# Kernel tuning notes

Hardware: AMD Instinct MI355X
Metric: run time of the kernel (lower is better)

## Reference

```python
import jax, jax.numpy as jnp
import numpy as np

D_MODEL = 1024
NUM_HEADS = 16
WINDOW = 128
DEPTH = D_MODEL // NUM_HEADS


def setup_inputs() -> dict:
    key = jax.random.key(0)
    ks = jax.random.split(key, 9)
    B, S = 2, 2048
    scale = 1.0 / np.sqrt(D_MODEL)
    x = jax.random.normal(ks[0], (B, S, D_MODEL), dtype=jnp.float32)
    Wq = jax.random.normal(ks[1], (D_MODEL, D_MODEL), dtype=jnp.float32) * scale
    Wk = jax.random.normal(ks[2], (D_MODEL, D_MODEL), dtype=jnp.float32) * scale
    Wv = jax.random.normal(ks[3], (D_MODEL, D_MODEL), dtype=jnp.float32) * scale
    Wo = jax.random.normal(ks[4], (D_MODEL, D_MODEL), dtype=jnp.float32) * scale
    bq = jnp.zeros((D_MODEL,), jnp.float32)
    bk = jnp.zeros((D_MODEL,), jnp.float32)
    bv = jnp.zeros((D_MODEL,), jnp.float32)
    bo = jnp.zeros((D_MODEL,), jnp.float32)
    return {"x": x, "Wq": Wq, "bq": bq, "Wk": Wk, "bk": bk,
            "Wv": Wv, "bv": bv, "Wo": Wo, "bo": bo}


def _split_heads(t, B, S):
    # [B,S,D] -> [B,H,S,depth]
    return t.reshape(B, S, NUM_HEADS, DEPTH).transpose(0, 2, 1, 3)


def reference(x, Wq, bq, Wk, bk, Wv, bv, Wo, bo):
    B, S, _ = x.shape
    q = _split_heads(x @ Wq + bq, B, S)
    k = _split_heads(x @ Wk + bk, B, S)
    v = _split_heads(x @ Wv + bv, B, S)
    scores = jnp.einsum('bhqd,bhkd->bhqk', q, k) / jnp.sqrt(jnp.float32(DEPTH))
    idx = jnp.arange(S)
    # mask[i_row=j, i_col=i] per original: |i - j| <= window (symmetric)
    local = jnp.abs(idx[None, :] - idx[:, None]) <= WINDOW  # [S,S]
    scores = jnp.where(local[None, None], scores, jnp.float32(-1e9))
    attn = jax.nn.softmax(scores, axis=-1)
    out = jnp.einsum('bhqk,bhkd->bhqd', attn, v)
    concat = out.transpose(0, 2, 1, 3).reshape(B, S, D_MODEL)
    return concat @ Wo + bo
```

## Files before the change

kernel.cpp:

```cpp
#include <hip/hip_runtime.h>
#include <cstdint>
#include <cstddef>

typedef __attribute__((ext_vector_type(8))) short short8;
typedef __attribute__((ext_vector_type(4))) short short4v;
typedef __attribute__((ext_vector_type(4))) float f32x4;
typedef short8 bf16x8;

typedef __attribute__((address_space(1))) const unsigned GU;
typedef __attribute__((address_space(3))) unsigned LU;

__device__ __forceinline__ short f2bf(float f) {
  unsigned u = __builtin_bit_cast(unsigned, f);
  u += 0x7fffu + ((u >> 16) & 1u);
  return (short)(u >> 16);
}

__global__ __launch_bounds__(256) void k_cast_x(const float* __restrict__ x, short* __restrict__ xb) {
  size_t i = ((size_t)blockIdx.x * 256 + threadIdx.x) * 8;
  f32x4 a = *(const f32x4*)(x + i);
  f32x4 b = *(const f32x4*)(x + i + 4);
  short8 o;
#pragma unroll
  for (int j = 0; j < 4; ++j) { o[j] = f2bf(a[j]); o[4 + j] = f2bf(b[j]); }
  *(short8*)(xb + i) = o;
}

__global__ __launch_bounds__(256) void k_tw(const float* __restrict__ W0, const float* __restrict__ W1,
                                            const float* __restrict__ W2, const float* __restrict__ W3,
                                            short* __restrict__ WT) {
  __shared__ short T[64 * 72];
  int bid = blockIdx.x;
  int widx = bid >> 8;
  int t = bid & 255;
  int kr = (t >> 4) * 64, nc = (t & 15) * 64;
  const float* W = widx == 0 ? W0 : widx == 1 ? W1 : widx == 2 ? W2 : W3;
  short* out = WT + (size_t)widx * 1048576;
  int tid = threadIdx.x;
#pragma unroll
  for (int i = 0; i < 4; ++i) {
    int idx = tid + i * 256;
    int k = idx >> 4, n4 = (idx & 15) << 2;
    f32x4 v = *(const f32x4*)(W + (size_t)(kr + k) * 1024 + nc + n4);
#pragma unroll
    for (int j = 0; j < 4; ++j) T[(n4 + j) * 72 + k] = f2bf(v[j]);
  }
  __syncthreads();
#pragma unroll
  for (int i = 0; i < 2; ++i) {
    int idx = tid + i * 256;
    int n = idx >> 3, k8 = (idx & 7) << 3;
    *(short8*)(out + (size_t)(nc + n) * 1024 + kr + k8) = *(const short8*)&T[n * 72 + k8];
  }
}

__global__ __launch_bounds__(256) void k_tv(const short* __restrict__ v, short* __restrict__ vT) {
  __shared__ short T[64 * 72];
  int bid = blockIdx.x;
  int stile = bid & 31, h = (bid >> 5) & 15, b = bid >> 9;
  int s0 = stile * 64;
  int tid = threadIdx.x;
#pragma unroll
  for (int i = 0; i < 2; ++i) {
    int idx = tid + i * 256;
    int s = idx >> 3, d0 = (idx & 7) << 3;
    short8 vec = *(const short8*)(v + ((size_t)b * 2048 + s0 + s) * 1024 + h * 64 + d0);
#pragma unroll
    for (int j = 0; j < 8; ++j) T[(d0 + j) * 72 + s] = vec[j];
  }
  __syncthreads();
#pragma unroll
  for (int i = 0; i < 2; ++i) {
    int idx = tid + i * 256;
    int d = idx >> 3, s8 = (idx & 7) << 3;
    *(short8*)(vT + (((size_t)b * 16 + h) * 64 + d) * 2048 + s0 + s8) = *(const short8*)&T[d * 72 + s8];
  }
}

__global__ __launch_bounds__(512, 2) void k_gemm256(
    const short* __restrict__ A, const short* __restrict__ BT,
    const float* __restrict__ bias0, const float* __restrict__ bias1, const float* __restrict__ bias2,
    short* __restrict__ outb) {
  __shared__ short S[65536];
  const int tid = threadIdx.x;
  const int lane = tid & 63, w = tid >> 6;
  const int g = lane >> 4, qi = lane & 15;
  const int wm = w >> 2, wn = w & 3;
  int bid = blockIdx.x;
  int swz = (bid & 7) * 24 + (bid >> 3);
  const int tm = swz / 12, tn = swz % 12;
  const int m0 = tm * 256, n0 = tn * 256;
  const size_t K = 1024;
  const short* Ab = A + (size_t)m0 * K;
  const short* Bb = BT + (size_t)n0 * K;

  auto stage = [&](int roff, const short* gbase, int kt) {
#pragma unroll
    for (int i = 0; i < 2; ++i) {
      int cc = tid + i * 512;
      int r = cc >> 3;
      int js = ((cc & 7) ^ (r & 7)) << 3;
      __builtin_amdgcn_global_load_lds((GU*)(gbase + (size_t)r * K + kt * 64 + js),
                                       (LU*)(&S[roff + cc * 8]), 16, 0, 0);
    }
  };
  auto lda = [&](int roff, int row, int kk) -> bf16x8 {
    return *(const bf16x8*)&S[roff + row * 64 + (((kk * 4 + g) ^ (row & 7)) << 3)];
  };

  f32x4 acc[8][4];
#pragma unroll
  for (int i = 0; i < 8; ++i)
#pragma unroll
    for (int j = 0; j < 4; ++j) acc[i][j] = (f32x4)(0.0f);

#define MFA(mi, ni, av, bv) \
  acc[mi][ni] = __builtin_amdgcn_mfma_f32_16x16x32_bf16(av, bv, acc[mi][ni], 0, 0, 0)
#define MF16(Aa, Bb_, o) \
  MFA((o)+0,0,(Aa)[(o)+0],(Bb_)[0]); MFA((o)+0,1,(Aa)[(o)+0],(Bb_)[1]); \
  MFA((o)+0,2,(Aa)[(o)+0],(Bb_)[2]); MFA((o)+0,3,(Aa)[(o)+0],(Bb_)[3]); \
  MFA((o)+1,0,(Aa)[(o)+1],(Bb_)[0]); MFA((o)+1,1,(Aa)[(o)+1],(Bb_)[1]); \
  MFA((o)+1,2,(Aa)[(o)+1],(Bb_)[2]); MFA((o)+1,3,(Aa)[(o)+1],(Bb_)[3]); \
  MFA((o)+2,0,(Aa)[(o)+2],(Bb_)[0]); MFA((o)+2,1,(Aa)[(o)+2],(Bb_)[1]); \
  MFA((o)+2,2,(Aa)[(o)+2],(Bb_)[2]); MFA((o)+2,3,(Aa)[(o)+2],(Bb_)[3]); \
  MFA((o)+3,0,(Aa)[(o)+3],(Bb_)[0]); MFA((o)+3,1,(Aa)[(o)+3],(Bb_)[1]); \
  MFA((o)+3,2,(Aa)[(o)+3],(Bb_)[2]); MFA((o)+3,3,(Aa)[(o)+3],(Bb_)[3])
#define SB __builtin_amdgcn_sched_barrier(0)
#define PHASE_TAIL(MFMAS) do { \
    SB; \
    __builtin_amdgcn_s_barrier(); \
    asm volatile("s_waitcnt lgkmcnt(0)" ::: "memory"); \
    SB; \
    __builtin_amdgcn_s_setprio(1); \
    MFMAS; \
    __builtin_amdgcn_s_setprio(0); \
    SB; \
    __builtin_amdgcn_s_barrier(); \
  } while (0)

  stage(0,     Ab,          0);
  stage(8192,  Ab + 131072, 0);
  stage(16384, Bb,          0);
  stage(24576, Bb + 131072, 0);
  stage(49152, Bb,          1);
  stage(57344, Bb + 131072, 1);
  asm volatile("s_waitcnt vmcnt(4)" ::: "memory");
  __builtin_amdgcn_s_barrier();

  for (int t = 0; t < 16; ++t) {
    const int b = t & 1, nb = b ^ 1;
    const int rA = b * 32768 + wm * 8192;
    const int rB = b * 32768 + 16384 + (wn >> 1) * 8192;
    const int brow = (wn & 1) * 64;
    const int t1 = t + 1 < 15 ? t + 1 : 15;
    const int t2 = t + 2 < 15 ? t + 2 : 15;
    bf16x8 aA[8], aB[4], cA[8], cB[4];

#pragma unroll
    for (int mf = 0; mf < 4; ++mf) aA[mf] = lda(rA, mf * 16 + qi, 0);
#pragma unroll
    for (int nf = 0; nf < 4; ++nf) aB[nf] = lda(rB, brow + nf * 16 + qi, 0);
    stage(nb * 32768, Ab, t1);
    PHASE_TAIL(MF16(aA, aB, 0));
#pragma unroll
    for (int mf = 4; mf < 8; ++mf) aA[mf] = lda(rA, mf * 16 + qi, 0);
#pragma unroll
    for (int nf = 0; nf < 4; ++nf) cB[nf] = lda(rB, brow + nf * 16 + qi, 1);
    stage(nb * 32768 + 8192, Ab + 131072, t1);
    PHASE_TAIL(MF16(aA, aB, 4));
#pragma unroll
    for (int mf = 0; mf < 4; ++mf) cA[mf] = lda(rA, mf * 16 + qi, 1);
    stage(b * 32768 + 16384, Bb, t2);
    PHASE_TAIL(MF16(cA, cB, 0));
#pragma unroll
    for (int mf = 4; mf < 8; ++mf) cA[mf] = lda(rA, mf * 16 + qi, 1);
    stage(b * 32768 + 24576, Bb + 131072, t2);
    asm volatile("s_waitcnt vmcnt(4)" ::: "memory");
    PHASE_TAIL(MF16(cA, cB, 4));
  }
#undef PHASE_TAIL
#undef MF16
#undef MFA
#undef SB

  asm volatile("s_waitcnt vmcnt(0)" ::: "memory");
  __syncthreads();
  int sel = n0 >> 10;
  const float* bias = sel == 0 ? bias0 : (sel == 1 ? bias1 : bias2);
  size_t outoff = (size_t)sel * 4194304;
  int ncol0 = n0 & 1023;
  float bv[4];
#pragma unroll
  for (int nf = 0; nf < 4; ++nf) bv[nf] = bias[ncol0 + wn * 64 + nf * 16 + qi];
  short* Ep = S;
#pragma unroll
  for (int p = 0; p < 2; ++p) {
    __syncthreads();
    if (wm == p) {
#pragma unroll
      for (int mf = 0; mf < 8; ++mf)
#pragma unroll
        for (int nf = 0; nf < 4; ++nf)
#pragma unroll
          for (int j = 0; j < 4; ++j)
            Ep[(mf * 16 + g * 4 + j) * 264 + wn * 64 + nf * 16 + qi] =
                f2bf(acc[mf][nf][j] + bv[nf]);
    }
    __syncthreads();
#pragma unroll
    for (int i = 0; i < 8; ++i) {
      int idx = tid + i * 512;
      int r = idx >> 5, c8 = (idx & 31) << 3;
      int grow = m0 + p * 128 + r;
      *(short8*)&outb[outoff + (size_t)grow * 1024 + ncol0 + c8] = *(const short8*)&Ep[r * 264 + c8];
    }
  }
}

__global__ __launch_bounds__(256, 2) void k_gemmO(
    const short* __restrict__ A, const short* __restrict__ BT,
    const float* __restrict__ bias0, float* __restrict__ outf) {
  __shared__ short Smem[16384];
  const int tid = threadIdx.x;
  const int lane = tid & 63, w = tid >> 6;
  const int g = lane >> 4, qi = lane & 15;
  const int wr = (w >> 1) * 64, wc = (w & 1) * 64;
  const int m0 = blockIdx.y * 128, n0 = blockIdx.x * 128;
  const size_t K = 1024;
  const short* Ab = A + (size_t)m0 * K;
  const short* Bb = BT + (size_t)n0 * K;

  auto stage = [&](int buf, int k0) {
    short* Asb = Smem + buf * 4096;
    short* Bsb = Smem + 8192 + buf * 4096;
#pragma unroll
    for (int i = 0; i < 2; ++i) {
      int cidx = tid + i * 256;
      int r = cidx >> 2;
      int csw = ((cidx & 3) ^ ((r >> 1) & 3)) << 3;
      __builtin_amdgcn_global_load_lds((GU*)(Ab + (size_t)r * K + k0 + csw),
                                       (LU*)(&Asb[cidx * 8]), 16, 0, 0);
      __builtin_amdgcn_global_load_lds((GU*)(Bb + (size_t)r * K + k0 + csw),
                                       (LU*)(&Bsb[cidx * 8]), 16, 0, 0);
    }
  };

  f32x4 acc[4][4];
#pragma unroll
  for (int i = 0; i < 4; ++i)
#pragma unroll
    for (int j = 0; j < 4; ++j) acc[i][j] = (f32x4)(0.0f);

  stage(0, 0);
  __syncthreads();
  for (int kt = 0; kt < 32; ++kt) {
    int cur = kt & 1;
    if (kt < 31) stage(cur ^ 1, (kt + 1) * 32);
    const short* Asb = Smem + cur * 4096;
    const short* Bsb = Smem + 8192 + cur * 4096;
    bf16x8 a[4], b[4];
#pragma unroll
    for (int mf = 0; mf < 4; ++mf) {
      int R = wr + mf * 16 + qi;
      a[mf] = *(const bf16x8*)&Asb[R * 32 + ((g ^ ((R >> 1) & 3)) << 3)];
    }
#pragma unroll
    for (int nf = 0; nf < 4; ++nf) {
      int R = wc + nf * 16 + qi;
      b[nf] = *(const bf16x8*)&Bsb[R * 32 + ((g ^ ((R >> 1) & 3)) << 3)];
    }
#pragma unroll
    for (int mf = 0; mf < 4; ++mf)
#pragma unroll
      for (int nf = 0; nf < 4; ++nf)
        acc[mf][nf] = __builtin_amdgcn_mfma_f32_16x16x32_bf16(a[mf], b[nf], acc[mf][nf], 0, 0, 0);
    __syncthreads();
  }

  float* Ft = (float*)Smem;
  float bv[4];
#pragma unroll
  for (int nf = 0; nf < 4; ++nf) bv[nf] = bias0[n0 + wc + nf * 16 + qi];
#pragma unroll
  for (int mf = 0; mf < 4; ++mf) {
    __syncthreads();
#pragma unroll
    for (int nf = 0; nf < 4; ++nf)
#pragma unroll
      for (int j = 0; j < 4; ++j)
        Ft[((w >> 1) * 16 + g * 4 + j) * 136 + wc + nf * 16 + qi] = acc[mf][nf][j] + bv[nf];
    __syncthreads();
#pragma unroll
    for (int i = 0; i < 4; ++i) {
      int idx = tid + i * 256;
      int r = idx >> 5, c4 = (idx & 31) << 2;
      int row = m0 + ((r >> 4) << 6) + mf * 16 + (r & 15);
      *(f32x4*)&outf[(size_t)row * 1024 + n0 + c4] = *(const f32x4*)&Ft[r * 136 + c4];
    }
  }
}

__global__ __launch_bounds__(256, 2) void k_attn(const short* __restrict__ qg_,
                                                 const short* __restrict__ kg_,
                                                 const short* __restrict__ vT,
                                                 short* __restrict__ outp) {
  __shared__ short Qs[64 * 72];
  __shared__ short Ks[64 * 72];
  __shared__ short Vs[64 * 72];
  __shared__ short Ps[4][16 * 72];
  int bid = blockIdx.x;
  int qt = bid & 31, h = (bid >> 5) & 15, b = bid >> 9;
  int q0 = qt * 64;
  int tid = threadIdx.x, lane = tid & 63, w = tid >> 6;
  int g = lane >> 4, qi = lane & 15;

  const short* qsrc = qg_ + ((size_t)b * 2048 + q0) * 1024 + h * 64;
#pragma unroll
  for (int i = 0; i < 2; ++i) {
    int idx = tid + i * 256;
    int r = idx >> 3, c = (idx & 7) << 3;
    *(short8*)&Qs[r * 72 + c] = *(const short8*)&qsrc[(size_t)r * 1024 + c];
  }

  float m = -1e30f, l = 0.f;
  f32x4 oacc[4];
#pragma unroll
  for (int i = 0; i < 4; ++i) oacc[i] = (f32x4)(0.0f);
  int qglob = q0 + w * 16 + qi;

  for (int cc = 0; cc < 5; ++cc) {
    int kb0 = q0 - 128 + cc * 64;
    if (kb0 < 0 || kb0 >= 2048) continue;
    __syncthreads();
    const short* ksrc = kg_ + ((size_t)b * 2048 + kb0) * 1024 + h * 64;
    const short* vsrc = vT + ((size_t)(b * 16 + h)) * 64 * 2048 + kb0;
#pragma unroll
    for (int i = 0; i < 2; ++i) {
      int idx = tid + i * 256;
      int r = idx >> 3, c = (idx & 7) << 3;
      *(short8*)&Ks[r * 72 + c] = *(const short8*)&ksrc[(size_t)r * 1024 + c];
      *(short8*)&Vs[r * 72 + c] = *(const short8*)&vsrc[(size_t)r * 2048 + c];
    }
    __syncthreads();

    f32x4 st[4];
#pragma unroll
    for (int i = 0; i < 4; ++i) st[i] = (f32x4)(0.0f);
#pragma unroll
    for (int ds = 0; ds < 2; ++ds) {
      bf16x8 qf = *(const bf16x8*)&Qs[(w * 16 + qi) * 72 + ds * 32 + g * 8];
#pragma unroll
      for (int mf = 0; mf < 4; ++mf) {
        bf16x8 kf = *(const bf16x8*)&Ks[(mf * 16 + qi) * 72 + ds * 32 + g * 8];
        st[mf] = __builtin_amdgcn_mfma_f32_16x16x32_bf16(kf, qf, st[mf], 0, 0, 0);
      }
    }

    float pv[16];
    float pm = -1e30f;
#pragma unroll
    for (int mf = 0; mf < 4; ++mf)
#pragma unroll
      for (int j = 0; j < 4; ++j) {
        int kcol = kb0 + mf * 16 + g * 4 + j;
        float s = st[mf][j] * 0.125f;
        int d = kcol - qglob;
        bool valid = (d >= -128) && (d <= 128);
        s = valid ? s : -1e30f;
        pv[mf * 4 + j] = s;
        pm = fmaxf(pm, s);
      }
    pm = fmaxf(pm, __shfl_xor(pm, 16));
    pm = fmaxf(pm, __shfl_xor(pm, 32));
    float mnew = fmaxf(m, pm);
    float scale = __expf(m - mnew);
    float ls = 0.f;
#pragma unroll
    for (int e = 0; e < 16; ++e) {
      float p = pv[e] > -1e29f ? __expf(pv[e] - mnew) : 0.f;
      pv[e] = p;
      ls += p;
    }
    ls += __shfl_xor(ls, 16);
    ls += __shfl_xor(ls, 32);
    l = l * scale + ls;
    m = mnew;
#pragma unroll
    for (int mf = 0; mf < 4; ++mf) oacc[mf] *= scale;

#pragma unroll
    for (int f = 0; f < 4; ++f) {
      short4v pk;
#pragma unroll
      for (int j = 0; j < 4; ++j) pk[j] = f2bf(pv[f * 4 + j]);
      *(short4v*)&Ps[w][qi * 72 + f * 16 + g * 4] = pk;
    }

#pragma unroll
    for (int ks = 0; ks < 2; ++ks) {
      bf16x8 pf = *(const bf16x8*)&Ps[w][qi * 72 + ks * 32 + g * 8];
#pragma unroll
      for (int mf = 0; mf < 4; ++mf) {
        bf16x8 vf = *(const bf16x8*)&Vs[(mf * 16 + qi) * 72 + ks * 32 + g * 8];
        oacc[mf] = __builtin_amdgcn_mfma_f32_16x16x32_bf16(vf, pf, oacc[mf], 0, 0, 0);
      }
    }
  }

  __syncthreads();
  short* Os = Ks;
  float inv = 1.f / l;
#pragma unroll
  for (int mf = 0; mf < 4; ++mf) {
    short4v pk;
#pragma unroll
    for (int j = 0; j < 4; ++j) pk[j] = f2bf(oacc[mf][j] * inv);
    *(short4v*)&Os[(w * 16 + qi) * 72 + mf * 16 + g * 4] = pk;
  }
  __syncthreads();
  short* dst = outp + ((size_t)b * 2048 + q0) * 1024 + h * 64;
  int r = tid >> 2, c16 = (tid & 3) << 4;
  *(short8*)&dst[(size_t)r * 1024 + c16] = *(const short8*)&Os[r * 72 + c16];
  *(short8*)&dst[(size_t)r * 1024 + c16 + 8] = *(const short8*)&Os[r * 72 + c16 + 8];
}

extern "C" void kernel_launch(void* const* d_in, const int* in_sizes, int n_in,
                              void* d_out, int out_size, void* d_ws, size_t ws_size,
                              hipStream_t stream) {
  const float* x  = (const float*)d_in[0];
  const float* Wq = (const float*)d_in[1];
  const float* bq = (const float*)d_in[2];
  const float* Wk = (const float*)d_in[3];
  const float* bk = (const float*)d_in[4];
  const float* Wv = (const float*)d_in[5];
  const float* bv = (const float*)d_in[6];
  const float* Wo = (const float*)d_in[7];
  const float* bo = (const float*)d_in[8];

  short* ws = (short*)d_ws;
  short* xb       = ws;
  short* qkv      = ws + 4194304;
  short* vbuf     = qkv + 2 * 4194304;
  short* vT       = ws;
  short* attn_out = vbuf;
  short* WT       = ws + 4 * 4194304;

  k_cast_x<<<2048, 256, 0, stream>>>(x, xb);
  k_tw<<<1024, 256, 0, stream>>>(Wq, Wk, Wv, Wo, WT);
  k_gemm256<<<192, 512, 0, stream>>>(xb, WT, bq, bk, bv, qkv);
  k_tv<<<1024, 256, 0, stream>>>(vbuf, vT);
  k_attn<<<1024, 256, 0, stream>>>(qkv, qkv + 4194304, vT, attn_out);
  {
    dim3 grid(8, 32);
    k_gemmO<<<grid, 256, 0, stream>>>(attn_out, WT + 3 * 1048576, bo, (float*)d_out);
  }
}
```

Baseline: 91.32 us.

## Retile QKV GEMM to 256x192 tiles for 256 blocks and merge prep kernels

The fused QKV projection GEMM switches from 256x256 tiles (192 blocks) to 256x192 tiles (256 blocks), so the grid fills all 256 CUs on MI355X. Staging is reworked into 64-row chunks, and each wave now holds a 128x48 accumulator. The epilogue picks the Q/K/V output buffer per column. The x cast and weight transpose kernels are merged into one launch to cut launch overhead. The trade-off is lower arithmetic intensity per tile and tiles that cross Q/K/V boundaries.

```diff
diff --git a/kernel.cpp b/kernel.cpp
--- a/kernel.cpp
+++ b/kernel.cpp
@@ -16,27 +16,29 @@
   return (short)(u >> 16);
 }
 
-__global__ __launch_bounds__(256) void k_cast_x(const float* __restrict__ x, short* __restrict__ xb) {
-  size_t i = ((size_t)blockIdx.x * 256 + threadIdx.x) * 8;
-  f32x4 a = *(const f32x4*)(x + i);
-  f32x4 b = *(const f32x4*)(x + i + 4);
-  short8 o;
-#pragma unroll
-  for (int j = 0; j < 4; ++j) { o[j] = f2bf(a[j]); o[4 + j] = f2bf(b[j]); }
-  *(short8*)(xb + i) = o;
-}
-
-__global__ __launch_bounds__(256) void k_tw(const float* __restrict__ W0, const float* __restrict__ W1,
-                                            const float* __restrict__ W2, const float* __restrict__ W3,
-                                            short* __restrict__ WT) {
+__global__ __launch_bounds__(256) void k_prep(const float* __restrict__ x,
+                                              const float* __restrict__ W0, const float* __restrict__ W1,
+                                              const float* __restrict__ W2, const float* __restrict__ W3,
+                                              short* __restrict__ xb, short* __restrict__ WT) {
   __shared__ short T[64 * 72];
   int bid = blockIdx.x;
+  int tid = threadIdx.x;
+  if (bid < 2048) {
+    size_t i = ((size_t)bid * 256 + tid) * 8;
+    f32x4 a = *(const f32x4*)(x + i);
+    f32x4 b = *(const f32x4*)(x + i + 4);
+    short8 o;
+#pragma unroll
+    for (int j = 0; j < 4; ++j) { o[j] = f2bf(a[j]); o[4 + j] = f2bf(b[j]); }
+    *(short8*)(xb + i) = o;
+    return;
+  }
+  bid -= 2048;
   int widx = bid >> 8;
   int t = bid & 255;
   int kr = (t >> 4) * 64, nc = (t & 15) * 64;
   const float* W = widx == 0 ? W0 : widx == 1 ? W1 : widx == 2 ? W2 : W3;
   short* out = WT + (size_t)widx * 1048576;
-  int tid = threadIdx.x;
 #pragma unroll
   for (int i = 0; i < 4; ++i) {
     int idx = tid + i * 256;
@@ -77,54 +79,53 @@
   }
 }
 
-__global__ __launch_bounds__(512, 2) void k_gemm256(
+__global__ __launch_bounds__(512, 1) void k_gemm256(
     const short* __restrict__ A, const short* __restrict__ BT,
     const float* __restrict__ bias0, const float* __restrict__ bias1, const float* __restrict__ bias2,
     short* __restrict__ outb) {
-  __shared__ short S[65536];
+  __shared__ short S[57344];
   const int tid = threadIdx.x;
   const int lane = tid & 63, w = tid >> 6;
   const int g = lane >> 4, qi = lane & 15;
   const int wm = w >> 2, wn = w & 3;
   int bid = blockIdx.x;
-  int swz = (bid & 7) * 24 + (bid >> 3);
-  const int tm = swz / 12, tn = swz % 12;
-  const int m0 = tm * 256, n0 = tn * 256;
+  int swz = (bid & 7) * 32 + (bid >> 3);
+  const int tm = swz >> 4, tn = swz & 15;
+  const int m0 = tm * 256, n0 = tn * 192;
   const size_t K = 1024;
   const short* Ab = A + (size_t)m0 * K;
   const short* Bb = BT + (size_t)n0 * K;
 
-  auto stage = [&](int roff, const short* gbase, int kt) {
-#pragma unroll
-    for (int i = 0; i < 2; ++i) {
-      int cc = tid + i * 512;
-      int r = cc >> 3;
-      int js = ((cc & 7) ^ (r & 7)) << 3;
-      __builtin_amdgcn_global_load_lds((GU*)(gbase + (size_t)r * K + kt * 64 + js),
-                                       (LU*)(&S[roff + cc * 8]), 16, 0, 0);
-    }
+  auto stage64 = [&](int roff, const short* gbase, int kt) {
+    int r = tid >> 3;
+    int js = ((tid & 7) ^ (r & 7)) << 3;
+    __builtin_amdgcn_global_load_lds((GU*)(gbase + (size_t)r * K + kt * 64 + js),
+                                     (LU*)(&S[roff + tid * 8]), 16, 0, 0);
   };
-  auto lda = [&](int roff, int row, int kk) -> bf16x8 {
-    return *(const bf16x8*)&S[roff + row * 64 + (((kk * 4 + g) ^ (row & 7)) << 3)];
+  auto lda_a = [&](int bbase, int mf, int kk) -> bf16x8 {
+    int row = (mf & 3) * 16 + qi;
+    int reg = wm * 2 + (mf >> 2);
+    return *(const bf16x8*)&S[bbase + reg * 4096 + row * 64 + (((kk * 4 + g) ^ (row & 7)) << 3)];
   };
-
-  f32x4 acc[8][4];
+  auto lda_b = [&](int bbase, int nf, int kk) -> bf16x8 {
+    int c = wn * 48 + nf * 16 + qi;
+    int reg = c >> 6, row = c & 63;
+    return *(const bf16x8*)&S[bbase + 16384 + reg * 4096 + row * 64 + (((kk * 4 + g) ^ (row & 7)) << 3)];
+  };
+
+  f32x4 acc[8][3];
 #pragma unroll
   for (int i = 0; i < 8; ++i)
 #pragma unroll
-    for (int j = 0; j < 4; ++j) acc[i][j] = (f32x4)(0.0f);
+    for (int j = 0; j < 3; ++j) acc[i][j] = (f32x4)(0.0f);
 
 #define MFA(mi, ni, av, bv) \
   acc[mi][ni] = __builtin_amdgcn_mfma_f32_16x16x32_bf16(av, bv, acc[mi][ni], 0, 0, 0)
-#define MF16(Aa, Bb_, o) \
-  MFA((o)+0,0,(Aa)[(o)+0],(Bb_)[0]); MFA((o)+0,1,(Aa)[(o)+0],(Bb_)[1]); \
-  MFA((o)+0,2,(Aa)[(o)+0],(Bb_)[2]); MFA((o)+0,3,(Aa)[(o)+0],(Bb_)[3]); \
-  MFA((o)+1,0,(Aa)[(o)+1],(Bb_)[0]); MFA((o)+1,1,(Aa)[(o)+1],(Bb_)[1]); \
-  MFA((o)+1,2,(Aa)[(o)+1],(Bb_)[2]); MFA((o)+1,3,(Aa)[(o)+1],(Bb_)[3]); \
-  MFA((o)+2,0,(Aa)[(o)+2],(Bb_)[0]); MFA((o)+2,1,(Aa)[(o)+2],(Bb_)[1]); \
-  MFA((o)+2,2,(Aa)[(o)+2],(Bb_)[2]); MFA((o)+2,3,(Aa)[(o)+2],(Bb_)[3]); \
-  MFA((o)+3,0,(Aa)[(o)+3],(Bb_)[0]); MFA((o)+3,1,(Aa)[(o)+3],(Bb_)[1]); \
-  MFA((o)+3,2,(Aa)[(o)+3],(Bb_)[2]); MFA((o)+3,3,(Aa)[(o)+3],(Bb_)[3])
+#define MF12(Aa, Bb_, o) \
+  MFA((o)+0,0,(Aa)[(o)+0],(Bb_)[0]); MFA((o)+0,1,(Aa)[(o)+0],(Bb_)[1]); MFA((o)+0,2,(Aa)[(o)+0],(Bb_)[2]); \
+  MFA((o)+1,0,(Aa)[(o)+1],(Bb_)[0]); MFA((o)+1,1,(Aa)[(o)+1],(Bb_)[1]); MFA((o)+1,2,(Aa)[(o)+1],(Bb_)[2]); \
+  MFA((o)+2,0,(Aa)[(o)+2],(Bb_)[0]); MFA((o)+2,1,(Aa)[(o)+2],(Bb_)[1]); MFA((o)+2,2,(Aa)[(o)+2],(Bb_)[2]); \
+  MFA((o)+3,0,(Aa)[(o)+3],(Bb_)[0]); MFA((o)+3,1,(Aa)[(o)+3],(Bb_)[1]); MFA((o)+3,2,(Aa)[(o)+3],(Bb_)[2])
 #define SB __builtin_amdgcn_sched_barrier(0)
 #define PHASE_TAIL(MFMAS) do { \
     SB; \
@@ -138,60 +139,69 @@
     __builtin_amdgcn_s_barrier(); \
   } while (0)
 
-  stage(0,     Ab,          0);
-  stage(8192,  Ab + 131072, 0);
-  stage(16384, Bb,          0);
-  stage(24576, Bb + 131072, 0);
-  stage(49152, Bb,          1);
-  stage(57344, Bb + 131072, 1);
-  asm volatile("s_waitcnt vmcnt(4)" ::: "memory");
+  stage64(0,     Ab,            0);
+  stage64(4096,  Ab + 65536,    0);
+  stage64(8192,  Ab + 131072,   0);
+  stage64(12288, Ab + 196608,   0);
+  stage64(16384, Bb,            0);
+  stage64(20480, Bb + 65536,    0);
+  stage64(24576, Bb + 131072,   0);
+  stage64(28672 + 16384, Bb,          1);
+  stage64(28672 + 20480, Bb + 65536,  1);
+  stage64(28672 + 24576, Bb + 131072, 1);
+  asm volatile("s_waitcnt vmcnt(3)" ::: "memory");
   __builtin_amdgcn_s_barrier();
 
   for (int t = 0; t < 16; ++t) {
     const int b = t & 1, nb = b ^ 1;
-    const int rA = b * 32768 + wm * 8192;
-    const int rB = b * 32768 + 16384 + (wn >> 1) * 8192;
-    const int brow = (wn & 1) * 64;
+    const int bb = b * 28672, nbb = nb * 28672;
     const int t1 = t + 1 < 15 ? t + 1 : 15;
     const int t2 = t + 2 < 15 ? t + 2 : 15;
-    bf16x8 aA[8], aB[4], cA[8], cB[4];
-
-#pragma unroll
-    for (int mf = 0; mf < 4; ++mf) aA[mf] = lda(rA, mf * 16 + qi, 0);
-#pragma unroll
-    for (int nf = 0; nf < 4; ++nf) aB[nf] = lda(rB, brow + nf * 16 + qi, 0);
-    stage(nb * 32768, Ab, t1);
-    PHASE_TAIL(MF16(aA, aB, 0));
-#pragma unroll
-    for (int mf = 4; mf < 8; ++mf) aA[mf] = lda(rA, mf * 16 + qi, 0);
-#pragma unroll
-    for (int nf = 0; nf < 4; ++nf) cB[nf] = lda(rB, brow + nf * 16 + qi, 1);
-    stage(nb * 32768 + 8192, Ab + 131072, t1);
-    PHASE_TAIL(MF16(aA, aB, 4));
-#pragma unroll
-    for (int mf = 0; mf < 4; ++mf) cA[mf] = lda(rA, mf * 16 + qi, 1);
-    stage(b * 32768 + 16384, Bb, t2);
-    PHASE_TAIL(MF16(cA, cB, 0));
-#pragma unroll
-    for (int mf = 4; mf < 8; ++mf) cA[mf] = lda(rA, mf * 16 + qi, 1);
-    stage(b * 32768 + 24576, Bb + 131072, t2);
-    asm volatile("s_waitcnt vmcnt(4)" ::: "memory");
-    PHASE_TAIL(MF16(cA, cB, 4));
+    bf16x8 aA[8], aB[3], cA[8], cB[3];
+
+#pragma unroll
+    for (int mf = 0; mf < 4; ++mf) aA[mf] = lda_a(bb, mf, 0);
+#pragma unroll
+    for (int nf = 0; nf < 3; ++nf) aB[nf] = lda_b(bb, nf, 0);
+    stage64(nbb,        Ab,         t1);
+    stage64(nbb + 4096, Ab + 65536, t1);
+    PHASE_TAIL(MF12(aA, aB, 0));
+#pragma unroll
+    for (int mf = 4; mf < 8; ++mf) aA[mf] = lda_a(bb, mf, 0);
+#pragma unroll
+    for (int nf = 0; nf < 3; ++nf) cB[nf] = lda_b(bb, nf, 1);
+    stage64(nbb + 8192,  Ab + 131072, t1);
+    stage64(nbb + 12288, Ab + 196608, t1);
+    PHASE_TAIL(MF12(aA, aB, 4));
+#pragma unroll
+    for (int mf = 0; mf < 4; ++mf) cA[mf] = lda_a(bb, mf, 1);
+    stage64(bb + 16384, Bb,         t2);
+    stage64(bb + 20480, Bb + 65536, t2);
+    PHASE_TAIL(MF12(cA, cB, 0));
+#pragma unroll
+    for (int mf = 4; mf < 8; ++mf) cA[mf] = lda_a(bb, mf, 1);
+    stage64(bb + 24576, Bb + 131072, t2);
+    asm volatile("s_waitcnt vmcnt(3)" ::: "memory");
+    PHASE_TAIL(MF12(cA, cB, 4));
   }
 #undef PHASE_TAIL
-#undef MF16
+#undef MF12
 #undef MFA
 #undef SB
 
   asm volatile("s_waitcnt vmcnt(0)" ::: "memory");
   __syncthreads();
-  int sel = n0 >> 10;
-  const float* bias = sel == 0 ? bias0 : (sel == 1 ? bias1 : bias2);
-  size_t outoff = (size_t)sel * 4194304;
-  int ncol0 = n0 & 1023;
-  float bv[4];
-#pragma unroll
-  for (int nf = 0; nf < 4; ++nf) bv[nf] = bias[ncol0 + wn * 64 + nf * 16 + qi];
+  float bv[3];
+  int seln[3];
+#pragma unroll
+  for (int nf = 0; nf < 3; ++nf) {
+    int colg = n0 + wn * 48 + nf * 16 + qi;
+    int sel = colg >> 10;
+    const float* bias = sel == 0 ? bias0 : (sel == 1 ? bias1 : bias2);
+    bv[nf] = bias[colg & 1023];
+    seln[nf] = sel;
+    (void)seln;
+  }
   short* Ep = S;
 #pragma unroll
   for (int p = 0; p < 2; ++p) {
@@ -200,19 +210,22 @@
 #pragma unroll
       for (int mf = 0; mf < 8; ++mf)
 #pragma unroll
-        for (int nf = 0; nf < 4; ++nf)
+        for (int nf = 0; nf < 3; ++nf)
 #pragma unroll
           for (int j = 0; j < 4; ++j)
-            Ep[(mf * 16 + g * 4 + j) * 264 + wn * 64 + nf * 16 + qi] =
+            Ep[(mf * 16 + g * 4 + j) * 200 + wn * 48 + nf * 16 + qi] =
                 f2bf(acc[mf][nf][j] + bv[nf]);
     }
     __syncthreads();
 #pragma unroll
-    for (int i = 0; i < 8; ++i) {
+    for (int i = 0; i < 6; ++i) {
       int idx = tid + i * 512;
-      int r = idx >> 5, c8 = (idx & 31) << 3;
+      int r = idx / 24, c8 = (idx % 24) * 8;
       int grow = m0 + p * 128 + r;
-      *(short8*)&outb[outoff + (size_t)grow * 1024 + ncol0 + c8] = *(const short8*)&Ep[r * 264 + c8];
+      int colg = n0 + c8;
+      int sel = colg >> 10;
+      *(short8*)&outb[(size_t)sel * 4194304 + (size_t)grow * 1024 + (colg & 1023)] =
+          *(const short8*)&Ep[r * 200 + c8];
     }
   }
 }
@@ -445,9 +458,8 @@
   short* attn_out = vbuf;
   short* WT       = ws + 4 * 4194304;
 
-  k_cast_x<<<2048, 256, 0, stream>>>(x, xb);
-  k_tw<<<1024, 256, 0, stream>>>(Wq, Wk, Wv, Wo, WT);
-  k_gemm256<<<192, 512, 0, stream>>>(xb, WT, bq, bk, bv, qkv);
+  k_prep<<<3072, 256, 0, stream>>>(x, Wq, Wk, Wv, Wo, xb, WT);
+  k_gemm256<<<256, 512, 0, stream>>>(xb, WT, bq, bk, bv, qkv);
   k_tv<<<1024, 256, 0, stream>>>(vbuf, vT);
   k_attn<<<1024, 256, 0, stream>>>(qkv, qkv + 4194304, vT, attn_out);
   {
```

New measurement: 87.21 us. -4.5%, faster.
